# Kernel tuning notes

Measured on AMD Instinct MI355X. Metric: run time of the kernel, lower is better.

Reference implementation:

```python
import jax, jax.numpy as jnp
import numpy as np

B, L, DIM, H = 2, 2048, 2048, 16
DH = DIM // H  # 128, size_per_head


def setup_inputs() -> dict:
    key = jax.random.key(0)
    k1, k2, k3, k4, k5, k6 = jax.random.split(key, 6)
    s = 0.02
    return {
        "query_tensor": jax.random.normal(k1, (B, L, DIM), jnp.float32),
        "value_tensor": jax.random.normal(k2, (B, L, DIM), jnp.float32),
        "attention_mask": jax.random.randint(k3, (B, L), 0, 2).astype(jnp.float32),
        "Wq": jax.random.normal(k4, (DIM, DIM), jnp.float32) * s,
        "Wk": jax.random.normal(k5, (DIM, DIM), jnp.float32) * s,
        "Wv": jax.random.normal(k6, (DIM, DIM), jnp.float32) * s,
    }


def reference(query_tensor, value_tensor, attention_mask, Wq, Wk, Wv):
    b, lq, dim = query_tensor.shape
    lv = value_tensor.shape[1]
    # torch Linear: x @ W.T (no bias)
    q = query_tensor @ Wq.T   # [B, Lq, DIM]
    k = value_tensor @ Wk.T   # [B, Lv, DIM]
    v = value_tensor @ Wv.T   # [B, Lv, DIM]
    # split heads -> [B, H, L, DH]
    q = q.reshape(b, lq, H, DH).transpose(0, 2, 1, 3)
    k = k.reshape(b, lv, H, DH).transpose(0, 2, 1, 3)
    v = v.reshape(b, lv, H, DH).transpose(0, 2, 1, 3)
    scores = jnp.einsum('bhqd,bhkd->bhqk', q, k) / jnp.sqrt(jnp.float32(DH))
    # multiplicative per-query mask, broadcast [B,1,Lq,1] -> [B,H,Lq,Lv]
    scores = scores * attention_mask[:, None, :, None]
    probs = jax.nn.softmax(scores, axis=-1)
    attn = jnp.einsum('bhqk,bhkd->bhqd', probs, v)  # [B,H,Lq,DH]
    return attn.transpose(0, 2, 1, 3).reshape(b, lq, dim)
```

## Files before the change

kernel.cpp:

```cpp
#include <hip/hip_runtime.h>
#include <hip/hip_bf16.h>
#include <stdint.h>

#define DIM_ 2048
#define L_   2048
#define B_   2
#define H_   16
#define DH_  128
#define NT_  32

#define QSCALE_ 0.12751743f

typedef __attribute__((ext_vector_type(4))) float fp32x4;
typedef __attribute__((ext_vector_type(8))) short s16x8;

__device__ __forceinline__ unsigned short bf16_rne(float f) {
    unsigned u = __builtin_bit_cast(unsigned, f);
    u += 0x7fffu + ((u >> 16) & 1u);
    return (unsigned short)(u >> 16);
}

__device__ __forceinline__ fp32x4 MFMA(s16x8 a, s16x8 b, fp32x4 c) {
    return __builtin_amdgcn_mfma_f32_16x16x32_bf16(a, b, c, 0, 0, 0);
}

__device__ __forceinline__ void gld16(const void* g, void* l) {
    auto gp = reinterpret_cast<const uint32_t __attribute__((address_space(1)))*>(
        reinterpret_cast<uintptr_t>(g));
    auto lp = reinterpret_cast<uint32_t __attribute__((address_space(3)))*>(
        reinterpret_cast<uintptr_t>(l));
    __builtin_amdgcn_global_load_lds(gp, lp, 16, 0, 0);
}

__device__ __forceinline__ float exp2_raw(float x) {
    float r; asm("v_exp_f32 %0, %1" : "=v"(r) : "v"(x)); return r;
}

__device__ __forceinline__ unsigned cvtpk_bf16(float a, float b) {
    unsigned r; asm("v_cvt_pk_bf16_f32 %0, %1, %2" : "=v"(r) : "v"(a), "v"(b)); return r;
}

__global__ void __launch_bounds__(256)
cvt_all(const float* __restrict__ query, const float* __restrict__ value,
        const float* __restrict__ Wq, const float* __restrict__ Wk,
        const float* __restrict__ Wv,
        unsigned short* __restrict__ qb, unsigned short* __restrict__ vb,
        unsigned short* __restrict__ wqb, unsigned short* __restrict__ wkb,
        unsigned short* __restrict__ wvb)
{
    const int total4 = 7340032;
    int i = blockIdx.x * 256 + threadIdx.x;
    const int stride = gridDim.x * 256;
    for (; i < total4; i += stride) {
        const float4* s; ushort4* d; int off; float sc = 1.0f;
        if (i < 2097152)      { s = (const float4*)query; d = (ushort4*)qb;  off = i; }
        else if (i < 4194304) { s = (const float4*)value; d = (ushort4*)vb;  off = i - 2097152; }
        else if (i < 5242880) { s = (const float4*)Wq;    d = (ushort4*)wqb; off = i - 4194304; sc = QSCALE_; }
        else if (i < 6291456) { s = (const float4*)Wk;    d = (ushort4*)wkb; off = i - 5242880; }
        else                  { s = (const float4*)Wv;    d = (ushort4*)wvb; off = i - 6291456; }
        float4 v = s[off];
        ushort4 o;
        o.x = bf16_rne(v.x * sc); o.y = bf16_rne(v.y * sc);
        o.z = bf16_rne(v.z * sc); o.w = bf16_rne(v.w * sc);
        d[off] = o;
    }
}

__global__ void __launch_bounds__(512, 2)
qgemm(const unsigned short* __restrict__ qb, const unsigned short* __restrict__ wqb,
      const float* __restrict__ mask, unsigned short* __restrict__ q_ws)
{
    __shared__ __align__(16) char As_[3][32768];
    __shared__ __align__(16) char Bs_[3][16384];

    const int tid  = threadIdx.x;
    const int lane = tid & 63;
    const int wid  = tid >> 6;
    const int wm   = wid >> 1;
    const int wn   = wid & 1;
    const int lr   = lane & 15;
    const int lg   = lane >> 4;

    const int rb = (blockIdx.x & 7) * 32 + (blockIdx.x >> 3);
    const int bm = (rb >> 4) << 8;
    const int bn = (rb & 15) << 7;

    const int srow = tid >> 3;
    const int scol = ((tid & 7) ^ ((tid >> 3) & 7)) * 8;
    const unsigned short* gA = qb  + (size_t)(bm + srow) * DIM_ + scol;
    const unsigned short* gB = wqb + (size_t)(bn + srow) * DIM_ + scol;
    const int ldst = wid * 1024;

    const int r7   = (lr & 7) << 4;
    const int arow = (wm * 64 + lr) * 128;
    const int brow = (wn * 64 + lr) * 128;
    const int off0 = (lg << 4) ^ r7;
    const int off1 = (64 | (lg << 4)) ^ r7;

    fp32x4 acc[4][4] = {};

#define STG6(SA, SB, T) do {                                                      \
    gld16(gA + (size_t)(T) * 64,                 (SA) + ldst);                    \
    gld16(gA + (size_t)64  * DIM_ + (T) * 64,    (SA) + 8192  + ldst);            \
    gld16(gA + (size_t)128 * DIM_ + (T) * 64,    (SA) + 16384 + ldst);            \
    gld16(gA + (size_t)192 * DIM_ + (T) * 64,    (SA) + 24576 + ldst);            \
    gld16(gB + (size_t)(T) * 64,                 (SB) + ldst);                    \
    gld16(gB + (size_t)64  * DIM_ + (T) * 64,    (SB) + 8192  + ldst);            \
} while (0)

    STG6(&As_[0][0], &Bs_[0][0], 0);
    STG6(&As_[1][0], &Bs_[1][0], 1);
    asm volatile("s_waitcnt vmcnt(6)" ::: "memory");
    __builtin_amdgcn_s_barrier();

    for (int t = 0; t < NT_; ++t) {
        char* Ab = &As_[t % 3][0];
        char* Bb = &Bs_[t % 3][0];
        if (t < NT_ - 2) {
            STG6(&As_[(t + 2) % 3][0], &Bs_[(t + 2) % 3][0], t + 2);
        }

        s16x8 fa0[4], fa1[4], fb0[4], fb1[4];
        #pragma unroll
        for (int mi = 0; mi < 4; ++mi) {
            fa0[mi] = *reinterpret_cast<const s16x8*>(&Ab[arow + mi * 2048 + off0]);
            fa1[mi] = *reinterpret_cast<const s16x8*>(&Ab[arow + mi * 2048 + off1]);
        }
        #pragma unroll
        for (int nf = 0; nf < 4; ++nf) {
            fb0[nf] = *reinterpret_cast<const s16x8*>(&Bb[brow + nf * 2048 + off0]);
            fb1[nf] = *reinterpret_cast<const s16x8*>(&Bb[brow + nf * 2048 + off1]);
        }

        __builtin_amdgcn_s_setprio(1);
        #pragma unroll
        for (int mi = 0; mi < 4; ++mi)
            #pragma unroll
            for (int nf = 0; nf < 4; ++nf)
                acc[mi][nf] = MFMA(fa0[mi], fb0[nf], acc[mi][nf]);
        #pragma unroll
        for (int mi = 0; mi < 4; ++mi)
            #pragma unroll
            for (int nf = 0; nf < 4; ++nf)
                acc[mi][nf] = MFMA(fa1[mi], fb1[nf], acc[mi][nf]);
        __builtin_amdgcn_s_setprio(0);

        if (t < NT_ - 2) {
            asm volatile("s_waitcnt vmcnt(6)" ::: "memory");
            __builtin_amdgcn_s_barrier();
        } else if (t == NT_ - 2) {
            asm volatile("s_waitcnt vmcnt(0)" ::: "memory");
            __builtin_amdgcn_s_barrier();
        }
    }
#undef STG6

    const int bb = bm >> 11;
    const size_t bh0 = (size_t)(bb * H_) * (L_ * DH_);
    const int rbase = bm + wm * 64;
    const int cbase = bn + wn * 64;
    const float* mrow = mask + bb * L_;

    #pragma unroll
    for (int mf = 0; mf < 4; ++mf)
        #pragma unroll
        for (int rr = 0; rr < 4; ++rr) {
            int l = (rbase + mf * 16 + lg * 4 + rr) & (L_ - 1);
            float mvv = mrow[l];
            #pragma unroll
            for (int nf = 0; nf < 4; ++nf) {
                int dc = cbase + nf * 16 + lr;
                int h = dc >> 7, d = dc & 127;
                q_ws[bh0 + (size_t)h * (L_ * DH_) + (size_t)l * DH_ + d]
                    = bf16_rne(acc[mf][nf][rr] * mvv);
            }
        }
}

__global__ void __launch_bounds__(512, 2)
kvgemm(const unsigned short* __restrict__ vb, const unsigned short* __restrict__ wkb,
       const unsigned short* __restrict__ wvb,
       unsigned short* __restrict__ k_ws, unsigned short* __restrict__ v_ws)
{
    __shared__ __align__(16) char As_[2][32768];
    __shared__ __align__(16) char Bks_[2][16384];
    __shared__ __align__(16) char Bvs_[2][16384];

    const int tid  = threadIdx.x;
    const int lane = tid & 63;
    const int wid  = tid >> 6;
    const int wm   = wid >> 1;
    const int wn   = wid & 1;
    const int lr   = lane & 15;
    const int lg   = lane >> 4;

    const int rb = (blockIdx.x & 7) * 32 + (blockIdx.x >> 3);
    const int bm = (rb >> 4) << 8;
    const int bn = (rb & 15) << 7;

    const int srow = tid >> 3;
    const int scol = ((tid & 7) ^ ((tid >> 3) & 7)) * 8;
    const unsigned short* gA  = vb  + (size_t)(bm + srow) * DIM_ + scol;
    const unsigned short* gBk = wkb + (size_t)(bn + srow) * DIM_ + scol;
    const unsigned short* gBv = wvb + (size_t)(bn + srow) * DIM_ + scol;
    const int ldst = wid * 1024;

    const int r7   = (lr & 7) << 4;
    const int arow = (wm * 64 + lr) * 128;
    const int brow = (wn * 64 + lr) * 128;
    const int off0 = (lg << 4) ^ r7;
    const int off1 = (64 | (lg << 4)) ^ r7;

    fp32x4 acck[4][4] = {};
    fp32x4 accv[4][4] = {};

#define STG8(BUF, T) do {                                                         \
    gld16(gA  + (size_t)(T) * 64,               &As_[BUF][ldst]);                 \
    gld16(gA  + (size_t)64  * DIM_ + (T) * 64,  &As_[BUF][8192  + ldst]);         \
    gld16(gA  + (size_t)128 * DIM_ + (T) * 64,  &As_[BUF][16384 + ldst]);         \
    gld16(gA  + (size_t)192 * DIM_ + (T) * 64,  &As_[BUF][24576 + ldst]);         \
    gld16(gBk + (size_t)(T) * 64,               &Bks_[BUF][ldst]);                \
    gld16(gBk + (size_t)64  * DIM_ + (T) * 64,  &Bks_[BUF][8192 + ldst]);         \
    gld16(gBv + (size_t)(T) * 64,               &Bvs_[BUF][ldst]);                \
    gld16(gBv + (size_t)64  * DIM_ + (T) * 64,  &Bvs_[BUF][8192 + ldst]);         \
} while (0)

    STG8(0, 0);
    asm volatile("s_waitcnt vmcnt(0)" ::: "memory");
    __builtin_amdgcn_s_barrier();

    for (int t = 0; t < NT_; ++t) {
        const int buf = t & 1;
        if (t + 1 < NT_) STG8(buf ^ 1, t + 1);

        char* Ab  = &As_[buf][0];
        char* Bkb = &Bks_[buf][0];
        char* Bvb = &Bvs_[buf][0];

        #pragma unroll
        for (int kk = 0; kk < 2; ++kk) {
            const int o = kk ? off1 : off0;
            s16x8 fa[4], fk[4];
            #pragma unroll
            for (int mi = 0; mi < 4; ++mi)
                fa[mi] = *reinterpret_cast<const s16x8*>(&Ab[arow + mi * 2048 + o]);
            #pragma unroll
            for (int nf = 0; nf < 4; ++nf)
                fk[nf] = *reinterpret_cast<const s16x8*>(&Bkb[brow + nf * 2048 + o]);
            __builtin_amdgcn_s_setprio(1);
            #pragma unroll
            for (int mi = 0; mi < 4; ++mi)
                #pragma unroll
                for (int nf = 0; nf < 4; ++nf)
                    acck[mi][nf] = MFMA(fa[mi], fk[nf], acck[mi][nf]);
            __builtin_amdgcn_s_setprio(0);
            s16x8 fv[4];
            #pragma unroll
            for (int nf = 0; nf < 4; ++nf)
                fv[nf] = *reinterpret_cast<const s16x8*>(&Bvb[brow + nf * 2048 + o]);
            __builtin_amdgcn_s_setprio(1);
            #pragma unroll
            for (int mi = 0; mi < 4; ++mi)
                #pragma unroll
                for (int nf = 0; nf < 4; ++nf)
                    accv[mi][nf] = MFMA(fa[mi], fv[nf], accv[mi][nf]);
            __builtin_amdgcn_s_setprio(0);
        }

        if (t + 1 < NT_) {
            asm volatile("s_waitcnt vmcnt(0)" ::: "memory");
            __builtin_amdgcn_s_barrier();
        }
    }
#undef STG8

    const int bb = bm >> 11;
    const size_t bh0 = (size_t)(bb * H_) * (L_ * DH_);
    const int rbase = bm + wm * 64;
    const int cbase = bn + wn * 64;

    #pragma unroll
    for (int mf = 0; mf < 4; ++mf)
        #pragma unroll
        for (int rr = 0; rr < 4; ++rr) {
            int l = (rbase + mf * 16 + lg * 4 + rr) & (L_ - 1);
            #pragma unroll
            for (int nf = 0; nf < 4; ++nf) {
                int dc = cbase + nf * 16 + lr;
                int h = dc >> 7, d = dc & 127;
                size_t off = bh0 + (size_t)h * (L_ * DH_)
                    + (size_t)(((l >> 4) * 4 + (d >> 5)) * 512
                    + ((l & 15) + (((d >> 3) & 3) << 4)) * 8 + (d & 7));
                k_ws[off] = bf16_rne(acck[mf][nf][rr]);
            }
        }

    #pragma unroll
    for (int mf = 0; mf < 4; ++mf) {
        int l0 = (rbase + mf * 16 + lg * 4) & (L_ - 1);
        #pragma unroll
        for (int nf = 0; nf < 4; ++nf) {
            int dc = cbase + nf * 16 + lr;
            int h = dc >> 7, d = dc & 127;
            size_t off = bh0 + (size_t)h * (L_ * DH_)
                + (size_t)(((l0 >> 5) * 8 + (d >> 4)) * 512
                + ((d & 15) + (((l0 >> 3) & 3) << 4)) * 8 + (l0 & 7));
            ushort4 pk;
            pk.x = bf16_rne(accv[mf][nf][0]);
            pk.y = bf16_rne(accv[mf][nf][1]);
            pk.z = bf16_rne(accv[mf][nf][2]);
            pk.w = bf16_rne(accv[mf][nf][3]);
            *reinterpret_cast<ushort4*>(&v_ws[off]) = pk;
        }
    }
}

__global__ void __launch_bounds__(256, 2)
attn_fused3(const unsigned short* __restrict__ qw, const unsigned short* __restrict__ kfr,
            const unsigned short* __restrict__ vfr, float* __restrict__ out)
{
    __shared__ __align__(16) char Ks[2][16384];
    __shared__ __align__(16) char Pl[4][4608];

    const int tid  = threadIdx.x;
    const int lane = tid & 63;
    const int wid  = tid >> 6;
    const int lr   = lane & 15;
    const int lg   = lane >> 4;

    const int p  = (blockIdx.x & 7) * 64 + (blockIdx.x >> 3);
    const int bh = p >> 4;
    const int qt = p & 15;
    const int b  = bh >> 4;
    const int h  = bh & 15;
    const int q0 = qt * 128 + wid * 32;

    const unsigned short* qbase = qw  + (size_t)bh * (L_ * DH_);
    const unsigned short* kbase = kfr + (size_t)bh * (L_ * DH_);
    const unsigned short* vbase = vfr + (size_t)bh * (L_ * DH_);

    s16x8 qf[2][4];
    #pragma unroll
    for (int qs = 0; qs < 2; ++qs)
        #pragma unroll
        for (int kc = 0; kc < 4; ++kc)
            qf[qs][kc] = *reinterpret_cast<const s16x8*>(
                &qbase[(size_t)(q0 + qs * 16 + lr) * DH_ + kc * 32 + lg * 8]);

    s16x8 ones;
    #pragma unroll
    for (int i = 0; i < 8; ++i) ones[i] = (short)0x3F80;

    fp32x4 acc[2][8] = {};
    fp32x4 racc[2] = {};

    char* P = &Pl[wid][0];

    auto STAGE = [&](int buf, int t) {
        const unsigned short* g = kbase + (size_t)t * 8192;
        #pragma unroll
        for (int c = 0; c < 4; ++c)
            gld16(g + c * 2048 + tid * 8, &Ks[buf][c * 4096 + wid * 1024]);
    };

    STAGE(0, 0);
    __syncthreads();

    for (int t = 0; t < L_ / 64; ++t) {
        const int buf = t & 1;
        if (t + 1 < L_ / 64) STAGE(buf ^ 1, t + 1);

        s16x8 vv0[8], vv1[8];
        #pragma unroll
        for (int ds = 0; ds < 8; ++ds)
            vv0[ds] = *reinterpret_cast<const s16x8*>(
                &vbase[(size_t)t * 8192 + (0 * 8 + ds) * 512 + lane * 8]);

        fp32x4 s2[2][4] = {};
        __builtin_amdgcn_s_setprio(1);
        #pragma unroll
        for (int kvs = 0; kvs < 4; ++kvs)
            #pragma unroll
            for (int kc = 0; kc < 4; ++kc) {
                s16x8 kf = *reinterpret_cast<const s16x8*>(
                    Ks[buf] + (kvs * 4 + kc) * 1024 + lane * 16);
                s2[0][kvs] = MFMA(kf, qf[0][kc], s2[0][kvs]);
                s2[1][kvs] = MFMA(kf, qf[1][kc], s2[1][kvs]);
            }
        __builtin_amdgcn_s_setprio(0);

        #pragma unroll
        for (int qs = 0; qs < 2; ++qs)
            #pragma unroll
            for (int kvs = 0; kvs < 4; ++kvs) {
                float e0 = exp2_raw(s2[qs][kvs][0]);
                float e1 = exp2_raw(s2[qs][kvs][1]);
                float e2 = exp2_raw(s2[qs][kvs][2]);
                float e3 = exp2_raw(s2[qs][kvs][3]);
                uint2 pk;
                pk.x = cvtpk_bf16(e0, e1);
                pk.y = cvtpk_bf16(e2, e3);
                *reinterpret_cast<uint2*>(P + qs * 2304 + lr * 144 + kvs * 32 + lg * 8) = pk;
            }

        #pragma unroll
        for (int ds = 0; ds < 8; ++ds)
            vv1[ds] = *reinterpret_cast<const s16x8*>(
                &vbase[(size_t)t * 8192 + (1 * 8 + ds) * 512 + lane * 8]);

        __builtin_amdgcn_s_setprio(1);
        #pragma unroll
        for (int qs = 0; qs < 2; ++qs) {
            s16x8 pa0 = *reinterpret_cast<const s16x8*>(P + qs * 2304 + lr * 144 + 0 * 64 + lg * 16);
            s16x8 pa1 = *reinterpret_cast<const s16x8*>(P + qs * 2304 + lr * 144 + 1 * 64 + lg * 16);
            racc[qs] = MFMA(pa0, ones, racc[qs]);
            racc[qs] = MFMA(pa1, ones, racc[qs]);
            #pragma unroll
            for (int ds = 0; ds < 8; ++ds) {
                acc[qs][ds] = MFMA(pa0, vv0[ds], acc[qs][ds]);
                acc[qs][ds] = MFMA(pa1, vv1[ds], acc[qs][ds]);
            }
        }
        __builtin_amdgcn_s_setprio(0);

        __syncthreads();
    }

    #pragma unroll
    for (int qs = 0; qs < 2; ++qs) {
        float inv[4];
        #pragma unroll
        for (int r = 0; r < 4; ++r) inv[r] = 1.0f / racc[qs][r];
        #pragma unroll
        for (int ds = 0; ds < 8; ++ds)
            #pragma unroll
            for (int r = 0; r < 4; ++r)
                out[((size_t)(b * L_ + q0 + qs * 16 + lg * 4 + r)) * DIM_ + h * DH_ + ds * 16 + lr]
                    = acc[qs][ds][r] * inv[r];
    }
}

extern "C" void kernel_launch(void* const* d_in, const int* in_sizes, int n_in,
                              void* d_out, int out_size, void* d_ws, size_t ws_size,
                              hipStream_t stream) {
    const float* query = (const float*)d_in[0];
    const float* value = (const float*)d_in[1];
    const float* mask  = (const float*)d_in[2];
    const float* Wq    = (const float*)d_in[3];
    const float* Wk    = (const float*)d_in[4];
    const float* Wv    = (const float*)d_in[5];
    float* out = (float*)d_out;

    const size_t elems  = (size_t)B_ * H_ * L_ * DH_;
    const size_t welems = elems / 2;
    unsigned short* q_ws = (unsigned short*)d_ws;
    unsigned short* k_ws = q_ws + elems;
    unsigned short* v_ws = k_ws + elems;

    unsigned short* qbf  = v_ws + elems;
    unsigned short* vbf  = qbf + elems;
    unsigned short* wqbf = vbf + elems;
    unsigned short* wkbf = wqbf + welems;
    unsigned short* wvbf = wkbf + welems;

    dim3 blk(256, 1, 1);

    cvt_all<<<dim3(2048, 1, 1), blk, 0, stream>>>(query, value, Wq, Wk, Wv,
                                                  qbf, vbf, wqbf, wkbf, wvbf);
    qgemm<<<dim3(256, 1, 1), dim3(512, 1, 1), 0, stream>>>(qbf, wqbf, mask, q_ws);
    kvgemm<<<dim3(256, 1, 1), dim3(512, 1, 1), 0, stream>>>(vbf, wkbf, wvbf, k_ws, v_ws);

    attn_fused3<<<dim3(512, 1, 1), blk, 0, stream>>>(q_ws, k_ws, v_ws, out);
}
```

Before: 194.1 us.

## Software-pipeline attention loop: overlap QK of next tile with softmax/PV of previous

New measurement: 194.6 us. About the same (+0.3%).

```diff
diff --git a/kernel.cpp b/kernel.cpp
--- a/kernel.cpp
+++ b/kernel.cpp
@@ -316,7 +316,7 @@
 }
 
 __global__ void __launch_bounds__(256, 2)
-attn_fused3(const unsigned short* __restrict__ qw, const unsigned short* __restrict__ kfr,
+attn_fused4(const unsigned short* __restrict__ qw, const unsigned short* __restrict__ kfr,
             const unsigned short* __restrict__ vfr, float* __restrict__ out)
 {
     __shared__ __align__(16) char Ks[2][16384];
@@ -353,6 +353,7 @@
 
     fp32x4 acc[2][8] = {};
     fp32x4 racc[2] = {};
+    fp32x4 sA[2][4], sB[2][4];
 
     char* P = &Pl[wid][0];
 
@@ -363,52 +364,41 @@
             gld16(g + c * 2048 + tid * 8, &Ks[buf][c * 4096 + wid * 1024]);
     };
 
-    STAGE(0, 0);
-    __syncthreads();
-
-    for (int t = 0; t < L_ / 64; ++t) {
-        const int buf = t & 1;
-        if (t + 1 < L_ / 64) STAGE(buf ^ 1, t + 1);
-
-        s16x8 vv0[8], vv1[8];
-        #pragma unroll
-        for (int ds = 0; ds < 8; ++ds)
-            vv0[ds] = *reinterpret_cast<const s16x8*>(
-                &vbase[(size_t)t * 8192 + (0 * 8 + ds) * 512 + lane * 8]);
-
-        fp32x4 s2[2][4] = {};
-        __builtin_amdgcn_s_setprio(1);
+    auto qk_tile = [&](int t, fp32x4 (&sc)[2][4]) {
+        char* kb = &Ks[t & 1][0];
+        #pragma unroll
+        for (int qs = 0; qs < 2; ++qs)
+            #pragma unroll
+            for (int kvs = 0; kvs < 4; ++kvs)
+                sc[qs][kvs] = fp32x4{0.f, 0.f, 0.f, 0.f};
         #pragma unroll
         for (int kvs = 0; kvs < 4; ++kvs)
             #pragma unroll
             for (int kc = 0; kc < 4; ++kc) {
                 s16x8 kf = *reinterpret_cast<const s16x8*>(
-                    Ks[buf] + (kvs * 4 + kc) * 1024 + lane * 16);
-                s2[0][kvs] = MFMA(kf, qf[0][kc], s2[0][kvs]);
-                s2[1][kvs] = MFMA(kf, qf[1][kc], s2[1][kvs]);
+                    kb + (kvs * 4 + kc) * 1024 + lane * 16);
+                sc[0][kvs] = MFMA(kf, qf[0][kc], sc[0][kvs]);
+                sc[1][kvs] = MFMA(kf, qf[1][kc], sc[1][kvs]);
             }
-        __builtin_amdgcn_s_setprio(0);
-
+    };
+
+    auto smax = [&](fp32x4 (&sp)[2][4]) {
         #pragma unroll
         for (int qs = 0; qs < 2; ++qs)
             #pragma unroll
             for (int kvs = 0; kvs < 4; ++kvs) {
-                float e0 = exp2_raw(s2[qs][kvs][0]);
-                float e1 = exp2_raw(s2[qs][kvs][1]);
-                float e2 = exp2_raw(s2[qs][kvs][2]);
-                float e3 = exp2_raw(s2[qs][kvs][3]);
+                float e0 = exp2_raw(sp[qs][kvs][0]);
+                float e1 = exp2_raw(sp[qs][kvs][1]);
+                float e2 = exp2_raw(sp[qs][kvs][2]);
+                float e3 = exp2_raw(sp[qs][kvs][3]);
                 uint2 pk;
                 pk.x = cvtpk_bf16(e0, e1);
                 pk.y = cvtpk_bf16(e2, e3);
                 *reinterpret_cast<uint2*>(P + qs * 2304 + lr * 144 + kvs * 32 + lg * 8) = pk;
             }
-
-        #pragma unroll
-        for (int ds = 0; ds < 8; ++ds)
-            vv1[ds] = *reinterpret_cast<const s16x8*>(
-                &vbase[(size_t)t * 8192 + (1 * 8 + ds) * 512 + lane * 8]);
-
-        __builtin_amdgcn_s_setprio(1);
+    };
+
+    auto pv = [&](s16x8 (&vv0)[8], s16x8 (&vv1)[8]) {
         #pragma unroll
         for (int qs = 0; qs < 2; ++qs) {
             s16x8 pa0 = *reinterpret_cast<const s16x8*>(P + qs * 2304 + lr * 144 + 0 * 64 + lg * 16);
@@ -421,9 +411,52 @@
                 acc[qs][ds] = MFMA(pa1, vv1[ds], acc[qs][ds]);
             }
         }
+    };
+
+    auto body = [&](int t, fp32x4 (&sc)[2][4], fp32x4 (&sp)[2][4]) {
+        if (t + 1 < NT_) STAGE((t + 1) & 1, t + 1);
+        s16x8 vv0[8], vv1[8];
+        const size_t vbt = (size_t)(t - 1) * 8192;
+        #pragma unroll
+        for (int ds = 0; ds < 8; ++ds)
+            vv0[ds] = *reinterpret_cast<const s16x8*>(&vbase[vbt + ds * 512 + lane * 8]);
+        #pragma unroll
+        for (int ds = 0; ds < 8; ++ds)
+            vv1[ds] = *reinterpret_cast<const s16x8*>(&vbase[vbt + (8 + ds) * 512 + lane * 8]);
+
+        smax(sp);
+
+        __builtin_amdgcn_s_setprio(1);
+        qk_tile(t, sc);
+        pv(vv0, vv1);
         __builtin_amdgcn_s_setprio(0);
 
         __syncthreads();
+    };
+
+    STAGE(0, 0);
+    __syncthreads();
+    STAGE(1, 1);
+    qk_tile(0, sA);
+    __syncthreads();
+
+    for (int t = 1; t + 1 < NT_; t += 2) {
+        body(t, sB, sA);
+        body(t + 1, sA, sB);
+    }
+    body(NT_ - 1, sB, sA);
+
+    {
+        s16x8 vv0[8], vv1[8];
+        const size_t vbt = (size_t)(NT_ - 1) * 8192;
+        #pragma unroll
+        for (int ds = 0; ds < 8; ++ds)
+            vv0[ds] = *reinterpret_cast<const s16x8*>(&vbase[vbt + ds * 512 + lane * 8]);
+        #pragma unroll
+        for (int ds = 0; ds < 8; ++ds)
+            vv1[ds] = *reinterpret_cast<const s16x8*>(&vbase[vbt + (8 + ds) * 512 + lane * 8]);
+        smax(sB);
+        pv(vv0, vv1);
     }
 
     #pragma unroll
@@ -470,5 +503,5 @@
     qgemm<<<dim3(256, 1, 1), dim3(512, 1, 1), 0, stream>>>(qbf, wqbf, mask, q_ws);
     kvgemm<<<dim3(256, 1, 1), dim3(512, 1, 1), 0, stream>>>(vbf, wkbf, wvbf, k_ws, v_ws);
 
-    attn_fused3<<<dim3(512, 1, 1), blk, 0, stream>>>(q_ws, k_ws, v_ws, out);
-}
+    attn_fused4<<<dim3(512, 1, 1), blk, 0, stream>>>(q_ws, k_ws, v_ws, out);
+}
```

## Load K fragments directly from global into registers, drop LDS staging and barrier

Applied to the files above, without the earlier changes.

Measured after the change: 205.6 us. 1.06x slower.

```diff
diff --git a/kernel.cpp b/kernel.cpp
--- a/kernel.cpp
+++ b/kernel.cpp
@@ -316,10 +316,9 @@
 }
 
 __global__ void __launch_bounds__(256, 2)
-attn_fused3(const unsigned short* __restrict__ qw, const unsigned short* __restrict__ kfr,
+attn_fused5(const unsigned short* __restrict__ qw, const unsigned short* __restrict__ kfr,
             const unsigned short* __restrict__ vfr, float* __restrict__ out)
 {
-    __shared__ __align__(16) char Ks[2][16384];
     __shared__ __align__(16) char Pl[4][4608];
 
     const int tid  = threadIdx.x;
@@ -356,25 +355,13 @@
 
     char* P = &Pl[wid][0];
 
-    auto STAGE = [&](int buf, int t) {
-        const unsigned short* g = kbase + (size_t)t * 8192;
-        #pragma unroll
-        for (int c = 0; c < 4; ++c)
-            gld16(g + c * 2048 + tid * 8, &Ks[buf][c * 4096 + wid * 1024]);
-    };
-
-    STAGE(0, 0);
-    __syncthreads();
-
-    for (int t = 0; t < L_ / 64; ++t) {
-        const int buf = t & 1;
-        if (t + 1 < L_ / 64) STAGE(buf ^ 1, t + 1);
-
-        s16x8 vv0[8], vv1[8];
-        #pragma unroll
-        for (int ds = 0; ds < 8; ++ds)
-            vv0[ds] = *reinterpret_cast<const s16x8*>(
-                &vbase[(size_t)t * 8192 + (0 * 8 + ds) * 512 + lane * 8]);
+    for (int t = 0; t < NT_; ++t) {
+        const size_t tb = (size_t)t * 8192;
+
+        s16x8 kf[16];
+        #pragma unroll
+        for (int i = 0; i < 16; ++i)
+            kf[i] = *reinterpret_cast<const s16x8*>(&kbase[tb + i * 512 + lane * 8]);
 
         fp32x4 s2[2][4] = {};
         __builtin_amdgcn_s_setprio(1);
@@ -382,12 +369,18 @@
         for (int kvs = 0; kvs < 4; ++kvs)
             #pragma unroll
             for (int kc = 0; kc < 4; ++kc) {
-                s16x8 kf = *reinterpret_cast<const s16x8*>(
-                    Ks[buf] + (kvs * 4 + kc) * 1024 + lane * 16);
-                s2[0][kvs] = MFMA(kf, qf[0][kc], s2[0][kvs]);
-                s2[1][kvs] = MFMA(kf, qf[1][kc], s2[1][kvs]);
+                s2[0][kvs] = MFMA(kf[kvs * 4 + kc], qf[0][kc], s2[0][kvs]);
+                s2[1][kvs] = MFMA(kf[kvs * 4 + kc], qf[1][kc], s2[1][kvs]);
             }
         __builtin_amdgcn_s_setprio(0);
+
+        s16x8 vv0[8], vv1[8];
+        #pragma unroll
+        for (int ds = 0; ds < 8; ++ds)
+            vv0[ds] = *reinterpret_cast<const s16x8*>(&vbase[tb + ds * 512 + lane * 8]);
+        #pragma unroll
+        for (int ds = 0; ds < 8; ++ds)
+            vv1[ds] = *reinterpret_cast<const s16x8*>(&vbase[tb + (8 + ds) * 512 + lane * 8]);
 
         #pragma unroll
         for (int qs = 0; qs < 2; ++qs)
@@ -403,11 +396,6 @@
                 *reinterpret_cast<uint2*>(P + qs * 2304 + lr * 144 + kvs * 32 + lg * 8) = pk;
             }
 
-        #pragma unroll
-        for (int ds = 0; ds < 8; ++ds)
-            vv1[ds] = *reinterpret_cast<const s16x8*>(
-                &vbase[(size_t)t * 8192 + (1 * 8 + ds) * 512 + lane * 8]);
-
         __builtin_amdgcn_s_setprio(1);
         #pragma unroll
         for (int qs = 0; qs < 2; ++qs) {
@@ -422,8 +410,6 @@
             }
         }
         __builtin_amdgcn_s_setprio(0);
-
-        __syncthreads();
     }
 
     #pragma unroll
@@ -470,5 +456,5 @@
     qgemm<<<dim3(256, 1, 1), dim3(512, 1, 1), 0, stream>>>(qbf, wqbf, mask, q_ws);
     kvgemm<<<dim3(256, 1, 1), dim3(512, 1, 1), 0, stream>>>(vbf, wkbf, wvbf, k_ws, v_ws);
 
-    attn_fused3<<<dim3(512, 1, 1), blk, 0, stream>>>(q_ws, k_ws, v_ws, out);
-}
+    attn_fused5<<<dim3(512, 1, 1), blk, 0, stream>>>(q_ws, k_ws, v_ws, out);
+}
```

## Double per-wave query rows in attention kernel to halve K/V reloads

Applied to the files above, without the earlier changes.

New measurement: 224.3 us. 15.6% more time.

```diff
diff --git a/kernel.cpp b/kernel.cpp
--- a/kernel.cpp
+++ b/kernel.cpp
@@ -315,12 +315,12 @@
     }
 }
 
-__global__ void __launch_bounds__(256, 2)
-attn_fused3(const unsigned short* __restrict__ qw, const unsigned short* __restrict__ kfr,
+__global__ void __launch_bounds__(256, 1)
+attn_fused6(const unsigned short* __restrict__ qw, const unsigned short* __restrict__ kfr,
             const unsigned short* __restrict__ vfr, float* __restrict__ out)
 {
     __shared__ __align__(16) char Ks[2][16384];
-    __shared__ __align__(16) char Pl[4][4608];
+    __shared__ __align__(16) char Pl[4][9216];
 
     const int tid  = threadIdx.x;
     const int lane = tid & 63;
@@ -328,20 +328,20 @@
     const int lr   = lane & 15;
     const int lg   = lane >> 4;
 
-    const int p  = (blockIdx.x & 7) * 64 + (blockIdx.x >> 3);
-    const int bh = p >> 4;
-    const int qt = p & 15;
+    const int p  = (blockIdx.x & 7) * 32 + (blockIdx.x >> 3);
+    const int bh = p >> 3;
+    const int qt = p & 7;
     const int b  = bh >> 4;
     const int h  = bh & 15;
-    const int q0 = qt * 128 + wid * 32;
+    const int q0 = qt * 256 + wid * 64;
 
     const unsigned short* qbase = qw  + (size_t)bh * (L_ * DH_);
     const unsigned short* kbase = kfr + (size_t)bh * (L_ * DH_);
     const unsigned short* vbase = vfr + (size_t)bh * (L_ * DH_);
 
-    s16x8 qf[2][4];
-    #pragma unroll
-    for (int qs = 0; qs < 2; ++qs)
+    s16x8 qf[4][4];
+    #pragma unroll
+    for (int qs = 0; qs < 4; ++qs)
         #pragma unroll
         for (int kc = 0; kc < 4; ++kc)
             qf[qs][kc] = *reinterpret_cast<const s16x8*>(
@@ -351,8 +351,8 @@
     #pragma unroll
     for (int i = 0; i < 8; ++i) ones[i] = (short)0x3F80;
 
-    fp32x4 acc[2][8] = {};
-    fp32x4 racc[2] = {};
+    fp32x4 acc[4][8] = {};
+    fp32x4 racc[4] = {};
 
     char* P = &Pl[wid][0];
 
@@ -366,60 +366,65 @@
     STAGE(0, 0);
     __syncthreads();
 
-    for (int t = 0; t < L_ / 64; ++t) {
+    for (int t = 0; t < NT_; ++t) {
         const int buf = t & 1;
-        if (t + 1 < L_ / 64) STAGE(buf ^ 1, t + 1);
-
-        s16x8 vv0[8], vv1[8];
+        if (t + 1 < NT_) STAGE(buf ^ 1, t + 1);
+        const size_t tb = (size_t)t * 8192;
+
+        s16x8 vv[8];
         #pragma unroll
         for (int ds = 0; ds < 8; ++ds)
-            vv0[ds] = *reinterpret_cast<const s16x8*>(
-                &vbase[(size_t)t * 8192 + (0 * 8 + ds) * 512 + lane * 8]);
-
-        fp32x4 s2[2][4] = {};
-        __builtin_amdgcn_s_setprio(1);
-        #pragma unroll
-        for (int kvs = 0; kvs < 4; ++kvs)
+            vv[ds] = *reinterpret_cast<const s16x8*>(&vbase[tb + ds * 512 + lane * 8]);
+
+        #pragma unroll
+        for (int kvs = 0; kvs < 4; ++kvs) {
+            fp32x4 s2[4] = {};
+            __builtin_amdgcn_s_setprio(1);
             #pragma unroll
             for (int kc = 0; kc < 4; ++kc) {
                 s16x8 kf = *reinterpret_cast<const s16x8*>(
                     Ks[buf] + (kvs * 4 + kc) * 1024 + lane * 16);
-                s2[0][kvs] = MFMA(kf, qf[0][kc], s2[0][kvs]);
-                s2[1][kvs] = MFMA(kf, qf[1][kc], s2[1][kvs]);
+                #pragma unroll
+                for (int qs = 0; qs < 4; ++qs)
+                    s2[qs] = MFMA(kf, qf[qs][kc], s2[qs]);
             }
-        __builtin_amdgcn_s_setprio(0);
-
-        #pragma unroll
-        for (int qs = 0; qs < 2; ++qs)
-            #pragma unroll
-            for (int kvs = 0; kvs < 4; ++kvs) {
-                float e0 = exp2_raw(s2[qs][kvs][0]);
-                float e1 = exp2_raw(s2[qs][kvs][1]);
-                float e2 = exp2_raw(s2[qs][kvs][2]);
-                float e3 = exp2_raw(s2[qs][kvs][3]);
+            __builtin_amdgcn_s_setprio(0);
+            #pragma unroll
+            for (int qs = 0; qs < 4; ++qs) {
+                float e0 = exp2_raw(s2[qs][0]);
+                float e1 = exp2_raw(s2[qs][1]);
+                float e2 = exp2_raw(s2[qs][2]);
+                float e3 = exp2_raw(s2[qs][3]);
                 uint2 pk;
                 pk.x = cvtpk_bf16(e0, e1);
                 pk.y = cvtpk_bf16(e2, e3);
                 *reinterpret_cast<uint2*>(P + qs * 2304 + lr * 144 + kvs * 32 + lg * 8) = pk;
             }
+        }
+
+        __builtin_amdgcn_s_setprio(1);
+        #pragma unroll
+        for (int qs = 0; qs < 4; ++qs) {
+            s16x8 pa = *reinterpret_cast<const s16x8*>(P + qs * 2304 + lr * 144 + lg * 16);
+            racc[qs] = MFMA(pa, ones, racc[qs]);
+            #pragma unroll
+            for (int ds = 0; ds < 8; ++ds)
+                acc[qs][ds] = MFMA(pa, vv[ds], acc[qs][ds]);
+        }
+        __builtin_amdgcn_s_setprio(0);
 
         #pragma unroll
         for (int ds = 0; ds < 8; ++ds)
-            vv1[ds] = *reinterpret_cast<const s16x8*>(
-                &vbase[(size_t)t * 8192 + (1 * 8 + ds) * 512 + lane * 8]);
+            vv[ds] = *reinterpret_cast<const s16x8*>(&vbase[tb + (8 + ds) * 512 + lane * 8]);
 
         __builtin_amdgcn_s_setprio(1);
         #pragma unroll
-        for (int qs = 0; qs < 2; ++qs) {
-            s16x8 pa0 = *reinterpret_cast<const s16x8*>(P + qs * 2304 + lr * 144 + 0 * 64 + lg * 16);
-            s16x8 pa1 = *reinterpret_cast<const s16x8*>(P + qs * 2304 + lr * 144 + 1 * 64 + lg * 16);
-            racc[qs] = MFMA(pa0, ones, racc[qs]);
-            racc[qs] = MFMA(pa1, ones, racc[qs]);
-            #pragma unroll
-            for (int ds = 0; ds < 8; ++ds) {
-                acc[qs][ds] = MFMA(pa0, vv0[ds], acc[qs][ds]);
-                acc[qs][ds] = MFMA(pa1, vv1[ds], acc[qs][ds]);
-            }
+        for (int qs = 0; qs < 4; ++qs) {
+            s16x8 pa = *reinterpret_cast<const s16x8*>(P + qs * 2304 + lr * 144 + 64 + lg * 16);
+            racc[qs] = MFMA(pa, ones, racc[qs]);
+            #pragma unroll
+            for (int ds = 0; ds < 8; ++ds)
+                acc[qs][ds] = MFMA(pa, vv[ds], acc[qs][ds]);
         }
         __builtin_amdgcn_s_setprio(0);
 
@@ -427,7 +432,7 @@
     }
 
     #pragma unroll
-    for (int qs = 0; qs < 2; ++qs) {
+    for (int qs = 0; qs < 4; ++qs) {
         float inv[4];
         #pragma unroll
         for (int r = 0; r < 4; ++r) inv[r] = 1.0f / racc[qs][r];
@@ -470,5 +475,5 @@
     qgemm<<<dim3(256, 1, 1), dim3(512, 1, 1), 0, stream>>>(qbf, wqbf, mask, q_ws);
     kvgemm<<<dim3(256, 1, 1), dim3(512, 1, 1), 0, stream>>>(vbf, wkbf, wvbf, k_ws, v_ws);
 
-    attn_fused3<<<dim3(512, 1, 1), blk, 0, stream>>>(q_ws, k_ws, v_ws, out);
-}
+    attn_fused6<<<dim3(256, 1, 1), blk, 0, stream>>>(q_ws, k_ws, v_ws, out);
+}
```
